# Kernel optimization log

Hardware: AMD Instinct MI355X
Metric: run time of the kernel (lower is better)

## Reference

```python
import jax, jax.numpy as jnp
import numpy as np

NUM_HEADS = 16
NUM_KV_HEADS = 8
HEAD_DIM = 128
GATE_LOW_RANK = 16
GATE_NORMALIZER = 16.0
NORM_EPS = 1e-5
CHUNK = 64


def gla_chunk(q, k, v, g, chunk=CHUNK):
    """Chunkwise-parallel gated linear attention.
    q,k,v,g: [B,H,L,D]. Recurrence: S_t = diag(exp(g_t)) S_{t-1} + k_t^T v_t; o_t = q_t S_t.
    """
    B, H, L, D = q.shape
    n = L // chunk

    def rs(x):  # -> [n, B, H, C, D]
        return x.reshape(B, H, n, chunk, D).transpose(2, 0, 1, 3, 4)

    qc, kc, vc, gc = rs(q), rs(k), rs(v), rs(g)
    causal = jnp.tril(jnp.ones((chunk, chunk), dtype=bool))

    def step(S, inp):
        qt, kt, vt, gt = inp                      # [B,H,C,D]
        b = jnp.cumsum(gt, axis=-2)               # inclusive cumulative log-gates
        q_ = qt * jnp.exp(b)
        k_ = kt * jnp.exp(-b)
        # intra-chunk causal attention (diag included)
        A = jnp.einsum('bhid,bhjd->bhij', q_, k_)
        A = jnp.where(causal, A, 0.0)
        o = jnp.einsum('bhij,bhje->bhie', A, vt)
        # inter-chunk contribution from carried state
        o = o + jnp.einsum('bhid,bhde->bhie', q_, S)
        # state update to end of chunk
        k_end = kt * jnp.exp(b[..., -1:, :] - b)
        S_new = S * jnp.exp(b[..., -1, :])[..., None] + jnp.einsum('bhcd,bhce->bhde', k_end, vt)
        return S_new, o

    S0 = jnp.zeros((B, H, D, D), q.dtype)
    _, o = jax.lax.scan(step, S0, (qc, kc, vc, gc))
    return o.transpose(1, 2, 0, 3, 4).reshape(B, H, L, D)


def setup_inputs() -> dict:
    key = jax.random.key(0)
    ks = jax.random.split(key, 10)
    B, L, HID = 2, 2048, 2048
    KV = NUM_KV_HEADS * HEAD_DIM  # 1024
    w = 0.02
    return {
        'hidden_states': jax.random.normal(ks[0], (B, L, HID), jnp.float32),
        'Wq': jax.random.normal(ks[1], (HID, HID), jnp.float32) * w,
        'bq': jnp.zeros((HID,), jnp.float32),
        'Wk': jax.random.normal(ks[2], (HID, KV), jnp.float32) * w,
        'bk': jnp.zeros((KV,), jnp.float32),
        'Wv': jax.random.normal(ks[3], (HID, KV), jnp.float32) * w,
        'bv': jnp.zeros((KV,), jnp.float32),
        'Wg1': jax.random.normal(ks[4], (HID, GATE_LOW_RANK), jnp.float32) * w,
        'Wg2': jax.random.normal(ks[5], (GATE_LOW_RANK, KV), jnp.float32) * w,
        'bg2': jnp.zeros((KV,), jnp.float32),
        'g_norm_w': jnp.ones((HEAD_DIM,), jnp.float32),
        'Wo': jax.random.normal(ks[6], (HID, HID), jnp.float32) * w,
    }


def reference(hidden_states, Wq, bq, Wk, bk, Wv, bv, Wg1, Wg2, bg2, g_norm_w, Wo):
    B, L, HID = hidden_states.shape
    H, HKV, D = NUM_HEADS, NUM_KV_HEADS, HEAD_DIM
    n_rep = H // HKV

    q = jax.nn.relu(hidden_states @ Wq + bq)          # feature_map = relu
    k = jax.nn.relu(hidden_states @ Wk + bk)
    v = hidden_states @ Wv + bv
    gk = jax.nn.log_sigmoid((hidden_states @ Wg1) @ Wg2 + bg2) / GATE_NORMALIZER

    q = q.reshape(B, L, H, D).transpose(0, 2, 1, 3)    # [B,H,L,D]
    def to_heads(x):
        return x.reshape(B, L, HKV, D).transpose(0, 2, 1, 3)
    k, v, gk = to_heads(k), to_heads(v), to_heads(gk)  # [B,HKV,L,D]
    # GQA: repeat kv heads
    k = jnp.repeat(k, n_rep, axis=1)
    v = jnp.repeat(v, n_rep, axis=1)
    gk = jnp.repeat(gk, n_rep, axis=1)

    q = q * (D ** -0.5)                                # scale as in chunk_gla
    o = gla_chunk(q, k, v, gk)                         # [B,H,L,D]

    # per-head RMSNorm over head_dim
    o = o * jax.lax.rsqrt(jnp.mean(o * o, axis=-1, keepdims=True) + NORM_EPS) * g_norm_w
    o = o.transpose(0, 2, 1, 3).reshape(B, L, H * D)
    return o @ Wo
```

## Files before the change

### kernel.cpp

```cpp
#include <hip/hip_runtime.h>

typedef unsigned short u16;
typedef u16 u16x8 __attribute__((ext_vector_type(8)));
typedef u16 u16x4 __attribute__((ext_vector_type(4)));
typedef __bf16 bf16x8 __attribute__((ext_vector_type(8)));
typedef float f32x4 __attribute__((ext_vector_type(4)));

#define DEVI static __device__ __forceinline__

DEVI float b2f(u16 u){ union { unsigned u; float f; } c; c.u = ((unsigned)u) << 16; return c.f; }
DEVI u16 f2b(float f){ union { float f; unsigned u; } c; c.f = f;
  unsigned r = c.u + 0x7fffu + ((c.u >> 16) & 1u); return (u16)(r >> 16); }
DEVI void gload16(const void* g, void* l){
  __builtin_amdgcn_global_load_lds((const __attribute__((address_space(1))) void*)g,
                                   (__attribute__((address_space(3))) void*)l, 16, 0, 0);
}
DEVI f32x4 MFMA(bf16x8 a, bf16x8 b, f32x4 c){
  return __builtin_amdgcn_mfma_f32_16x16x32_bf16(a, b, c, 0, 0, 0);
}

constexpr size_t OFF_HB  = 0;
constexpr size_t OFF_WCT = OFF_HB  + (size_t)4096*2048*2;
constexpr size_t OFF_WOT = OFF_WCT + (size_t)4224*2048*2;
constexpr size_t OFF_QKV = OFF_WOT + (size_t)2048*2048*2;
constexpr size_t OFF_G1  = OFF_QKV + (size_t)4096*4096*2;
constexpr size_t OFF_G   = OFF_G1  + (size_t)4096*16*4;
constexpr size_t OFF_EB  = OFF_G   + (size_t)4096*1024*4;
constexpr size_t OFF_KD  = OFF_EB  + (size_t)4096*1024*2;
constexpr size_t OFF_T   = OFF_KD  + (size_t)4096*1024*2;
constexpr size_t OFF_DV  = OFF_T   + (size_t)2*8*32*128*128*2;
constexpr size_t OFF_SP  = OFF_DV  + (size_t)2*8*32*128*4;
constexpr size_t OFF_ON  = OFF_SP  + (size_t)2*8*32*128*128*2;

__global__ __launch_bounds__(256) void k_conv_h(const float* __restrict__ h, u16* __restrict__ hb){
  int idx = blockIdx.x*256 + threadIdx.x, stride = gridDim.x*256;
  for (int i = idx; i < 4096*2048/4; i += stride){
    float4 v = ((const float4*)h)[i];
    u16x4 o; o[0]=f2b(v.x); o[1]=f2b(v.y); o[2]=f2b(v.z); o[3]=f2b(v.w);
    ((u16x4*)hb)[i] = o;
  }
}

__global__ __launch_bounds__(256) void k_transpose(const float* __restrict__ src, u16* __restrict__ dst,
                                                   int K, int N, int rowOff, int pitch){
  __shared__ float tile[64][65];
  int kb = blockIdx.y*64, nb = blockIdx.x*64;
  int t = threadIdx.x, x = t & 63, y0 = t >> 6;
#pragma unroll
  for (int i = 0; i < 16; i++){
    int y = y0 + i*4, k = kb + y, n = nb + x;
    tile[y][x] = (n < N) ? src[(size_t)k*N + n] : 0.f;
  }
  __syncthreads();
#pragma unroll
  for (int i = 0; i < 16; i++){
    int y = y0 + i*4, n = nb + y, k = kb + x;
    if (n < N) dst[(size_t)(rowOff + n)*pitch + k] = f2b(tile[x][y]);
  }
}

__global__ __launch_bounds__(256) void k_wtilde(const float* __restrict__ Wg1, const float* __restrict__ Wg2,
                                                u16* __restrict__ wt){
  __shared__ float w2s[16*8];
  int c0 = blockIdx.x*8, t = threadIdx.x;
  if (t < 128){ int j = t>>3, cc = t&7; w2s[j*8+cc] = Wg2[j*1024 + c0 + cc]; }
  __syncthreads();
  int r0 = t*8;
#pragma unroll
  for (int half = 0; half < 2; half++){
    float rowv[4][16];
#pragma unroll
    for (int u = 0; u < 4; u++)
#pragma unroll
      for (int j4 = 0; j4 < 4; j4++)
        *(float4*)&rowv[u][j4*4] = *(const float4*)&Wg1[(size_t)(r0 + half*4 + u)*16 + j4*4];
#pragma unroll
    for (int cc = 0; cc < 8; cc++){
      u16x4 o;
#pragma unroll
      for (int u = 0; u < 4; u++){
        float s = 0.f;
#pragma unroll
        for (int j = 0; j < 16; j++) s += rowv[u][j]*w2s[j*8+cc];
        o[u] = f2b(s);
      }
      *(u16x4*)&wt[(size_t)(c0+cc)*2048 + r0 + half*4] = o;
    }
  }
}

template<int MODE>
__global__ __launch_bounds__(256, 4) void gemm128(const u16* __restrict__ A, const u16* __restrict__ Bt,
                                                  u16* __restrict__ Cq, float* __restrict__ Cf,
                                                  const float* __restrict__ bq, const float* __restrict__ bk,
                                                  const float* __restrict__ bv, const float* __restrict__ bg2){
  constexpr int NT = 64;
  constexpr int NTN = (MODE==0) ? 32 : (MODE==1) ? 16 : 8;
  constexpr int CPX = (MODE==0) ? 128 : (MODE==1) ? 64 : 32;
  __shared__ u16 sA[2*128*32];
  __shared__ u16 sB[2*128*32];
  int id = blockIdx.x;
  int swz = (id & 7)*CPX + (id >> 3);
  int mt = swz / NTN, nt = swz % NTN;
  int t = threadIdx.x, w = t >> 6, l = t & 63;
  int wr = w >> 1, wc = w & 1;
  int mRow0 = mt*128, nCol0 = nt*128;
  const u16* srcA[2]; const u16* srcB[2];
#pragma unroll
  for (int i = 0; i < 2; i++){
    int S = t + i*256, r = S>>2, g = (S&3) ^ ((r>>1)&3);
    srcA[i] = A + (size_t)(mRow0 + r)*2048 + g*8;
    srcB[i] = Bt + (size_t)(nCol0 + r)*2048 + g*8;
  }
  auto ISSUE = [&](int T){
    int buf = T & 1;
    u16* dA = sA + buf*4096;
    u16* dB = sB + buf*4096;
#pragma unroll
    for (int i = 0; i < 2; i++) gload16(srcA[i] + T*32, dA + (i*256 + w*64)*8);
#pragma unroll
    for (int i = 0; i < 2; i++) gload16(srcB[i] + T*32, dB + (i*256 + w*64)*8);
  };
  f32x4 acc[4][4] = {};
  ISSUE(0);
  for (int T = 0; T < NT; ++T){
    __syncthreads();
    if (T + 1 < NT) ISSUE(T + 1);
    const u16* bufA = sA + (T&1)*4096;
    const u16* bufB = sB + (T&1)*4096;
    bf16x8 bfr[4], afr[4];
#pragma unroll
    for (int ni = 0; ni < 4; ni++){
      int r = wc*64 + ni*16 + (l&15);
      int p = (l>>4) ^ ((r>>1)&3);
      bfr[ni] = *(const bf16x8*)&bufB[(r*4 + p)*8];
    }
#pragma unroll
    for (int mi = 0; mi < 4; mi++){
      int r = wr*64 + mi*16 + (l&15);
      int p = (l>>4) ^ ((r>>1)&3);
      afr[mi] = *(const bf16x8*)&bufA[(r*4 + p)*8];
    }
    __builtin_amdgcn_s_setprio(1);
#pragma unroll
    for (int mi = 0; mi < 4; mi++)
#pragma unroll
      for (int ni = 0; ni < 4; ni++)
        acc[mi][ni] = MFMA(afr[mi], bfr[ni], acc[mi][ni]);
    __builtin_amdgcn_s_setprio(0);
  }
  int iLoc = (l>>4)*4, jc = l & 15;
  if (MODE == 0){
    int kind = (nt < 16) ? 0 : (nt < 24) ? 1 : 2;
#pragma unroll
    for (int ni = 0; ni < 4; ni++){
      int n = nCol0 + wc*64 + ni*16 + jc;
      float bias = (kind == 0) ? bq[n] : (kind == 1) ? bk[n - 2048] : bv[n - 3072];
#pragma unroll
      for (int mi = 0; mi < 4; mi++){
        int m = mRow0 + wr*64 + mi*16 + iLoc;
#pragma unroll
        for (int rr = 0; rr < 4; rr++){
          float x = acc[mi][ni][rr] + bias;
          int row = m + rr;
          if (kind == 0)      Cq[(size_t)row*4096 + n] = f2b(fmaxf(x, 0.f) * 0.08838834764831845f);
          else if (kind == 1) Cq[(size_t)row*4096 + n] = f2b(fmaxf(x, 0.f));
          else                Cq[(size_t)row*4096 + n] = f2b(x);
        }
      }
    }
  } else if (MODE == 1){
#pragma unroll
    for (int ni = 0; ni < 4; ni++){
      int n = nCol0 + wc*64 + ni*16 + jc;
#pragma unroll
      for (int mi = 0; mi < 4; mi++){
        int m = mRow0 + wr*64 + mi*16 + iLoc;
#pragma unroll
        for (int rr = 0; rr < 4; rr++) Cf[(size_t)(m+rr)*2048 + n] = acc[mi][ni][rr];
      }
    }
  } else {
#pragma unroll
    for (int ni = 0; ni < 4; ni++){
      int n = nCol0 + wc*64 + ni*16 + jc;
      float bias = bg2[n];
#pragma unroll
      for (int mi = 0; mi < 4; mi++){
        int m = mRow0 + wr*64 + mi*16 + iLoc;
#pragma unroll
        for (int rr = 0; rr < 4; rr++) Cf[(size_t)(m+rr)*1024 + n] = acc[mi][ni][rr] + bias;
      }
    }
  }
}

__global__ __launch_bounds__(256) void k_phaseA(const float* __restrict__ g, const u16* __restrict__ QKV,
                                                u16* __restrict__ eb, u16* __restrict__ kd,
                                                u16* __restrict__ T, float* __restrict__ Dv){
  __shared__ float gb[64*128];
  __shared__ u16 keT[128*72];
  __shared__ u16 vT [128*72];
  int c = blockIdx.x, kvh = blockIdx.y, b = blockIdx.z;
  int t = threadIdx.x;
  int tok0 = b*2048 + c*64;
#pragma unroll
  for (int r = 0; r < 8; r++){
    int idx4 = r*256 + t;
    int i = idx4 >> 5, c4 = idx4 & 31;
    float4 v = *(const float4*)&g[(size_t)(tok0+i)*1024 + kvh*128 + c4*4];
    float4 o;
    o.x = (fminf(v.x,0.f) - log1pf(expf(-fabsf(v.x)))) * 0.0625f;
    o.y = (fminf(v.y,0.f) - log1pf(expf(-fabsf(v.y)))) * 0.0625f;
    o.z = (fminf(v.z,0.f) - log1pf(expf(-fabsf(v.z)))) * 0.0625f;
    o.w = (fminf(v.w,0.f) - log1pf(expf(-fabsf(v.w)))) * 0.0625f;
    ((float4*)gb)[i*32 + c4] = o;
  }
  __syncthreads();
  if (t < 128){
    float run = 0.f;
    for (int i = 0; i < 64; i++){ run += gb[i*128 + t]; gb[i*128 + t] = run; }
    Dv[((size_t)(b*8+kvh)*32 + c)*128 + t] = expf(run);
  }
  __syncthreads();
  int d0 = (t&15)*8;
  float blast[8];
#pragma unroll
  for (int j = 0; j < 8; j++) blast[j] = gb[63*128 + d0 + j];
#pragma unroll
  for (int r = 0; r < 4; r++){
    int i = (t>>4) + r*16;
    u16x8 kv_ = *(const u16x8*)&QKV[(size_t)(tok0+i)*4096 + 2048 + kvh*128 + d0];
    u16x8 vv  = *(const u16x8*)&QKV[(size_t)(tok0+i)*4096 + 3072 + kvh*128 + d0];
    u16x8 ebv, kdv;
#pragma unroll
    for (int j = 0; j < 8; j++){
      float bcur = gb[i*128 + d0 + j];
      float kf = b2f(kv_[j]);
      ebv[j] = f2b(expf(bcur));
      kdv[j] = f2b(kf * expf(-bcur));
      keT[(d0+j)*72 + i] = f2b(kf * expf(blast[j] - bcur));
      vT [(d0+j)*72 + i] = vv[j];
    }
    *(u16x8*)&eb[(size_t)(tok0+i)*1024 + kvh*128 + d0] = ebv;
    *(u16x8*)&kd[(size_t)(tok0+i)*1024 + kvh*128 + d0] = kdv;
  }
  __syncthreads();
  int w = t>>6, l = t&63;
  f32x4 acc[2][8] = {};
#pragma unroll
  for (int ks = 0; ks < 2; ks++){
    bf16x8 af[2];
#pragma unroll
    for (int te = 0; te < 2; te++)
      af[te] = *(const bf16x8*)&vT[(w*32 + te*16 + (l&15))*72 + ks*32 + (l>>4)*8];
#pragma unroll
    for (int td = 0; td < 8; td++){
      bf16x8 bf_ = *(const bf16x8*)&keT[(td*16 + (l&15))*72 + ks*32 + (l>>4)*8];
#pragma unroll
      for (int te = 0; te < 2; te++) acc[te][td] = MFMA(af[te], bf_, acc[te][td]);
    }
  }
  size_t tbase = ((size_t)(b*8+kvh)*32 + c)*16384;
#pragma unroll
  for (int te = 0; te < 2; te++)
#pragma unroll
    for (int td = 0; td < 8; td++)
#pragma unroll
      for (int rr = 0; rr < 4; rr++){
        int e = w*32 + te*16 + (l>>4)*4 + rr, d = td*16 + (l&15);
        T[tbase + e*128 + d] = f2b(acc[te][td][rr]);
      }
}

__global__ __launch_bounds__(256) void k_phaseB(const u16* __restrict__ T, const float* __restrict__ Dv,
                                                u16* __restrict__ SP){
  int kvh = blockIdx.y, b = blockIdx.z;
  int t = threadIdx.x;
  int e = blockIdx.x*16 + (t >> 4);
  int d0 = (t & 15)*8;
  size_t base = ((size_t)(b*8 + kvh)*32)*16384 + (size_t)e*128 + d0;
  size_t dvb  = ((size_t)(b*8 + kvh)*32)*128 + d0;
  float S[8] = {0,0,0,0,0,0,0,0};
  for (int c = 0; c < 32; c++){
    u16x8 tv = *(const u16x8*)&T[base + (size_t)c*16384];
    float4 dva = *(const float4*)&Dv[dvb + (size_t)c*128];
    float4 dvbv = *(const float4*)&Dv[dvb + (size_t)c*128 + 4];
    u16x8 o;
#pragma unroll
    for (int j = 0; j < 8; j++) o[j] = f2b(S[j]);
    *(u16x8*)&SP[base + (size_t)c*16384] = o;
    float dv[8] = {dva.x, dva.y, dva.z, dva.w, dvbv.x, dvbv.y, dvbv.z, dvbv.w};
#pragma unroll
    for (int j = 0; j < 8; j++) S[j] = S[j]*dv[j] + b2f(tv[j]);
  }
}

__global__ __launch_bounds__(256) void k_phaseC(const u16* __restrict__ QKV, const u16* __restrict__ eb,
                                                const u16* __restrict__ kd, const u16* __restrict__ SP,
                                                const float* __restrict__ gnw, u16* __restrict__ onrm){
  __shared__ u16 kl[64*128];
  __shared__ u16 sl[64*72];
  __shared__ u16 vT[128*72];
  int c = blockIdx.x, h = blockIdx.y, b = blockIdx.z;
  int kvh = h >> 1;
  int t = threadIdx.x, w = t>>6, l = t&63;
  int tok0 = b*2048 + c*64;
#pragma unroll
  for (int is = 0; is < 4; is++){
    int row = (t>>4) + is*16;
    int d0s = 8*((t&15) ^ (row&7));
    gload16(&kd[(size_t)(tok0+row)*1024 + kvh*128 + d0s], &kl[is*2048 + w*512]);
  }
  int d0v = (t&15)*8;
#pragma unroll
  for (int r = 0; r < 4; r++){
    int i = (t>>4) + r*16;
    u16x8 vv = *(const u16x8*)&QKV[(size_t)(tok0+i)*4096 + 3072 + kvh*128 + d0v];
#pragma unroll
    for (int jj = 0; jj < 8; jj++) vT[(d0v+jj)*72 + i] = vv[jj];
  }
  bf16x8 aq[4];
  {
    int i = w*16 + (l&15);
#pragma unroll
    for (int kt = 0; kt < 4; kt++){
      int dq = kt*32 + (l>>4)*8;
      u16x8 qv = *(const u16x8*)&QKV[(size_t)(tok0+i)*4096 + h*128 + dq];
      u16x8 ev = *(const u16x8*)&eb[(size_t)(tok0+i)*1024 + kvh*128 + dq];
      u16x8 o;
#pragma unroll
      for (int jj = 0; jj < 8; jj++) o[jj] = f2b(b2f(qv[jj]) * b2f(ev[jj]));
      aq[kt] = __builtin_bit_cast(bf16x8, o);
    }
  }
  __syncthreads();
  f32x4 accs[4] = {};
#pragma unroll
  for (int kt = 0; kt < 4; kt++){
#pragma unroll
    for (int jt = 0; jt < 4; jt++){
      int j = jt*16 + (l&15);
      int byte_ = j*256 + ((2*(kt*32 + (l>>4)*8)) ^ ((j&7)<<4));
      bf16x8 bk_ = *(const bf16x8*)((const char*)kl + byte_);
      accs[jt] = MFMA(aq[kt], bk_, accs[jt]);
    }
  }
#pragma unroll
  for (int jt = 0; jt < 4; jt++)
#pragma unroll
    for (int rr = 0; rr < 4; rr++){
      int i = w*16 + (l>>4)*4 + rr;
      int j = jt*16 + (l&15);
      sl[i*72 + j] = f2b((i >= j) ? accs[jt][rr] : 0.f);
    }
  f32x4 acco[8] = {};
  size_t spb = ((size_t)(b*8+kvh)*32 + c)*16384;
#pragma unroll
  for (int kt = 0; kt < 4; kt++){
#pragma unroll
    for (int et = 0; et < 8; et++){
      int e = et*16 + (l&15);
      int dd = kt*32 + (l>>4)*8;
      bf16x8 bs = *(const bf16x8*)&SP[spb + (size_t)e*128 + dd];
      acco[et] = MFMA(aq[kt], bs, acco[et]);
    }
  }
#pragma unroll
  for (int kt2 = 0; kt2 < 2; kt2++){
    int i = w*16 + (l&15);
    bf16x8 as = *(const bf16x8*)&sl[i*72 + kt2*32 + (l>>4)*8];
#pragma unroll
    for (int et = 0; et < 8; et++){
      bf16x8 bv_ = *(const bf16x8*)&vT[(et*16 + (l&15))*72 + kt2*32 + (l>>4)*8];
      acco[et] = MFMA(as, bv_, acco[et]);
    }
  }
  float gw[8];
#pragma unroll
  for (int et = 0; et < 8; et++) gw[et] = gnw[et*16 + (l&15)];
#pragma unroll
  for (int rr = 0; rr < 4; rr++){
    int i = w*16 + (l>>4)*4 + rr;
    float ss = 0.f;
#pragma unroll
    for (int et = 0; et < 8; et++){ float x = acco[et][rr]; ss += x*x; }
    ss += __shfl_xor(ss, 1); ss += __shfl_xor(ss, 2);
    ss += __shfl_xor(ss, 4); ss += __shfl_xor(ss, 8);
    float sc = rsqrtf(ss*(1.f/128.f) + 1e-5f);
#pragma unroll
    for (int et = 0; et < 8; et++){
      int e = et*16 + (l&15);
      onrm[(size_t)(tok0+i)*2048 + h*128 + e] = f2b(acco[et][rr]*sc*gw[et]);
    }
  }
}

extern "C" void kernel_launch(void* const* d_in, const int* in_sizes, int n_in,
                              void* d_out, int out_size, void* d_ws, size_t ws_size,
                              hipStream_t stream){
  (void)in_sizes; (void)n_in; (void)out_size; (void)ws_size;
  const float* h   = (const float*)d_in[0];
  const float* Wq  = (const float*)d_in[1];
  const float* bq  = (const float*)d_in[2];
  const float* Wk  = (const float*)d_in[3];
  const float* bk  = (const float*)d_in[4];
  const float* Wv  = (const float*)d_in[5];
  const float* bv  = (const float*)d_in[6];
  const float* Wg1 = (const float*)d_in[7];
  const float* Wg2 = (const float*)d_in[8];
  const float* bg2 = (const float*)d_in[9];
  const float* gnw = (const float*)d_in[10];
  const float* Wo  = (const float*)d_in[11];
  float* out = (float*)d_out;
  char* ws = (char*)d_ws;
  u16*   hb   = (u16*)  (ws + OFF_HB);
  u16*   wct  = (u16*)  (ws + OFF_WCT);
  u16*   wot  = (u16*)  (ws + OFF_WOT);
  u16*   qkv  = (u16*)  (ws + OFF_QKV);
  float* gbuf = (float*)(ws + OFF_G);
  u16*   ebuf = (u16*)  (ws + OFF_EB);
  u16*   kdb  = (u16*)  (ws + OFF_KD);
  u16*   Tb   = (u16*)  (ws + OFF_T);
  u16*   wtilT= (u16*)  (ws + OFF_T);
  float* Dvb  = (float*)(ws + OFF_DV);
  u16*   SPb  = (u16*)  (ws + OFF_SP);
  u16*   onb  = (u16*)  (ws + OFF_ON);

  k_conv_h<<<2048, 256, 0, stream>>>(h, hb);
  k_transpose<<<dim3(32,32), 256, 0, stream>>>(Wq,  wct, 2048, 2048,    0, 2048);
  k_transpose<<<dim3(16,32), 256, 0, stream>>>(Wk,  wct, 2048, 1024, 2048, 2048);
  k_transpose<<<dim3(16,32), 256, 0, stream>>>(Wv,  wct, 2048, 1024, 3072, 2048);
  k_transpose<<<dim3(32,32), 256, 0, stream>>>(Wo,  wot, 2048, 2048,    0, 2048);
  k_wtilde<<<128, 256, 0, stream>>>(Wg1, Wg2, wtilT);
  gemm128<0><<<1024, 256, 0, stream>>>(hb, wct, qkv, nullptr, bq, bk, bv, nullptr);
  gemm128<2><<<256, 256, 0, stream>>>(hb, wtilT, nullptr, gbuf, nullptr, nullptr, nullptr, bg2);
  k_phaseA<<<dim3(32,8,2), 256, 0, stream>>>(gbuf, qkv, ebuf, kdb, Tb, Dvb);
  k_phaseB<<<dim3(8,8,2), 256, 0, stream>>>(Tb, Dvb, SPb);
  k_phaseC<<<dim3(32,16,2), 256, 0, stream>>>(qkv, ebuf, kdb, SPb, gnw, onb);
  gemm128<1><<<512, 256, 0, stream>>>(onb, wot, nullptr, out, nullptr, nullptr, nullptr, nullptr);
}
```

Before: 423.0 us.

## Fuse prep kernels, merge gate GEMM into QKV GEMM, share K/V across head pairs

Merges the bf16 conversion, the four weight transposes and the low-rank gate weight build into a single prep launch. Folds the gate projection GEMM into the QKV GEMM by adding extra N tiles that read from a separate weight buffer and write fp32 gates with bias. phaseC now runs one block per KV head and loops over both query heads, so the K/V tiles staged in shared memory are reused, at the cost of half as many blocks and extra barriers. Two serial loops also get unroll pragmas. The intent is fewer launches, better GEMM occupancy and less redundant K/V loading.

```diff
diff --git a/kernel.cpp b/kernel.cpp
--- a/kernel.cpp
+++ b/kernel.cpp
@@ -31,38 +31,48 @@
 constexpr size_t OFF_DV  = OFF_T   + (size_t)2*8*32*128*128*2;
 constexpr size_t OFF_SP  = OFF_DV  + (size_t)2*8*32*128*4;
 constexpr size_t OFF_ON  = OFF_SP  + (size_t)2*8*32*128*128*2;
-
-__global__ __launch_bounds__(256) void k_conv_h(const float* __restrict__ h, u16* __restrict__ hb){
-  int idx = blockIdx.x*256 + threadIdx.x, stride = gridDim.x*256;
-  for (int i = idx; i < 4096*2048/4; i += stride){
-    float4 v = ((const float4*)h)[i];
-    u16x4 o; o[0]=f2b(v.x); o[1]=f2b(v.y); o[2]=f2b(v.z); o[3]=f2b(v.w);
-    ((u16x4*)hb)[i] = o;
-  }
-}
-
-__global__ __launch_bounds__(256) void k_transpose(const float* __restrict__ src, u16* __restrict__ dst,
-                                                   int K, int N, int rowOff, int pitch){
+constexpr size_t OFF_WTL = OFF_ON  + (size_t)4096*2048*2;
+
+__global__ __launch_bounds__(256) void k_prep(const float* __restrict__ h, u16* __restrict__ hb,
+                                              const float* __restrict__ Wq, const float* __restrict__ Wk,
+                                              const float* __restrict__ Wv, const float* __restrict__ Wo,
+                                              u16* __restrict__ wct, u16* __restrict__ wot,
+                                              const float* __restrict__ Wg1, const float* __restrict__ Wg2,
+                                              u16* __restrict__ wt){
   __shared__ float tile[64][65];
-  int kb = blockIdx.y*64, nb = blockIdx.x*64;
-  int t = threadIdx.x, x = t & 63, y0 = t >> 6;
-#pragma unroll
-  for (int i = 0; i < 16; i++){
-    int y = y0 + i*4, k = kb + y, n = nb + x;
-    tile[y][x] = (n < N) ? src[(size_t)k*N + n] : 0.f;
-  }
-  __syncthreads();
-#pragma unroll
-  for (int i = 0; i < 16; i++){
-    int y = y0 + i*4, n = nb + y, k = kb + x;
-    if (n < N) dst[(size_t)(rowOff + n)*pitch + k] = f2b(tile[x][y]);
-  }
-}
-
-__global__ __launch_bounds__(256) void k_wtilde(const float* __restrict__ Wg1, const float* __restrict__ Wg2,
-                                                u16* __restrict__ wt){
+  int id = blockIdx.x, t = threadIdx.x;
+  if (id < 2048){
+    int idx = id*256 + t;
+    for (int i = idx; i < 4096*2048/4; i += 2048*256){
+      float4 v = ((const float4*)h)[i];
+      u16x4 o; o[0]=f2b(v.x); o[1]=f2b(v.y); o[2]=f2b(v.z); o[3]=f2b(v.w);
+      ((u16x4*)hb)[i] = o;
+    }
+    return;
+  }
+  if (id < 5120){
+    const float* src; u16* dst; int N, rowOff, bx, by;
+    if (id < 3072){ int lo = id-2048; src = Wq; dst = wct; N = 2048; rowOff = 0;    bx = lo&31; by = lo>>5; }
+    else if (id < 3584){ int lo = id-3072; src = Wk; dst = wct; N = 1024; rowOff = 2048; bx = lo&15; by = lo>>4; }
+    else if (id < 4096){ int lo = id-3584; src = Wv; dst = wct; N = 1024; rowOff = 3072; bx = lo&15; by = lo>>4; }
+    else { int lo = id-4096; src = Wo; dst = wot; N = 2048; rowOff = 0; bx = lo&31; by = lo>>5; }
+    int kb = by*64, nb = bx*64;
+    int x = t & 63, y0 = t >> 6;
+#pragma unroll
+    for (int i = 0; i < 16; i++){
+      int y = y0 + i*4;
+      tile[y][x] = src[(size_t)(kb + y)*N + nb + x];
+    }
+    __syncthreads();
+#pragma unroll
+    for (int i = 0; i < 16; i++){
+      int y = y0 + i*4;
+      dst[(size_t)(rowOff + nb + y)*2048 + kb + x] = f2b(tile[x][y]);
+    }
+    return;
+  }
   __shared__ float w2s[16*8];
-  int c0 = blockIdx.x*8, t = threadIdx.x;
+  int c0 = (id - 5120)*8;
   if (t < 128){ int j = t>>3, cc = t&7; w2s[j*8+cc] = Wg2[j*1024 + c0 + cc]; }
   __syncthreads();
   int r0 = t*8;
@@ -91,12 +101,13 @@
 
 template<int MODE>
 __global__ __launch_bounds__(256, 4) void gemm128(const u16* __restrict__ A, const u16* __restrict__ Bt,
+                                                  const u16* __restrict__ BtHi,
                                                   u16* __restrict__ Cq, float* __restrict__ Cf,
                                                   const float* __restrict__ bq, const float* __restrict__ bk,
                                                   const float* __restrict__ bv, const float* __restrict__ bg2){
   constexpr int NT = 64;
-  constexpr int NTN = (MODE==0) ? 32 : (MODE==1) ? 16 : 8;
-  constexpr int CPX = (MODE==0) ? 128 : (MODE==1) ? 64 : 32;
+  constexpr int NTN = (MODE==0) ? 40 : 16;
+  constexpr int CPX = (MODE==0) ? 160 : 64;
   __shared__ u16 sA[2*128*32];
   __shared__ u16 sB[2*128*32];
   int id = blockIdx.x;
@@ -105,12 +116,14 @@
   int t = threadIdx.x, w = t >> 6, l = t & 63;
   int wr = w >> 1, wc = w & 1;
   int mRow0 = mt*128, nCol0 = nt*128;
+  const u16* Bbase = (MODE==0 && nCol0 >= 4096) ? (BtHi + (size_t)(nCol0-4096)*2048)
+                                                : (Bt + (size_t)nCol0*2048);
   const u16* srcA[2]; const u16* srcB[2];
 #pragma unroll
   for (int i = 0; i < 2; i++){
     int S = t + i*256, r = S>>2, g = (S&3) ^ ((r>>1)&3);
     srcA[i] = A + (size_t)(mRow0 + r)*2048 + g*8;
-    srcB[i] = Bt + (size_t)(nCol0 + r)*2048 + g*8;
+    srcB[i] = Bbase + (size_t)r*2048 + g*8;
   }
   auto ISSUE = [&](int T){
     int buf = T & 1;
@@ -151,11 +164,12 @@
   }
   int iLoc = (l>>4)*4, jc = l & 15;
   if (MODE == 0){
-    int kind = (nt < 16) ? 0 : (nt < 24) ? 1 : 2;
+    int kind = (nt < 16) ? 0 : (nt < 24) ? 1 : (nt < 32) ? 2 : 3;
 #pragma unroll
     for (int ni = 0; ni < 4; ni++){
       int n = nCol0 + wc*64 + ni*16 + jc;
-      float bias = (kind == 0) ? bq[n] : (kind == 1) ? bk[n - 2048] : bv[n - 3072];
+      float bias = (kind == 0) ? bq[n] : (kind == 1) ? bk[n - 2048]
+                 : (kind == 2) ? bv[n - 3072] : bg2[n - 4096];
 #pragma unroll
       for (int mi = 0; mi < 4; mi++){
         int m = mRow0 + wr*64 + mi*16 + iLoc;
@@ -165,11 +179,12 @@
           int row = m + rr;
           if (kind == 0)      Cq[(size_t)row*4096 + n] = f2b(fmaxf(x, 0.f) * 0.08838834764831845f);
           else if (kind == 1) Cq[(size_t)row*4096 + n] = f2b(fmaxf(x, 0.f));
-          else                Cq[(size_t)row*4096 + n] = f2b(x);
+          else if (kind == 2) Cq[(size_t)row*4096 + n] = f2b(x);
+          else                Cf[(size_t)row*1024 + (n - 4096)] = x;
         }
       }
     }
-  } else if (MODE == 1){
+  } else {
 #pragma unroll
     for (int ni = 0; ni < 4; ni++){
       int n = nCol0 + wc*64 + ni*16 + jc;
@@ -178,18 +193,6 @@
         int m = mRow0 + wr*64 + mi*16 + iLoc;
 #pragma unroll
         for (int rr = 0; rr < 4; rr++) Cf[(size_t)(m+rr)*2048 + n] = acc[mi][ni][rr];
-      }
-    }
-  } else {
-#pragma unroll
-    for (int ni = 0; ni < 4; ni++){
-      int n = nCol0 + wc*64 + ni*16 + jc;
-      float bias = bg2[n];
-#pragma unroll
-      for (int mi = 0; mi < 4; mi++){
-        int m = mRow0 + wr*64 + mi*16 + iLoc;
-#pragma unroll
-        for (int rr = 0; rr < 4; rr++) Cf[(size_t)(m+rr)*1024 + n] = acc[mi][ni][rr] + bias;
       }
     }
   }
@@ -219,6 +222,7 @@
   __syncthreads();
   if (t < 128){
     float run = 0.f;
+#pragma unroll
     for (int i = 0; i < 64; i++){ run += gb[i*128 + t]; gb[i*128 + t] = run; }
     Dv[((size_t)(b*8+kvh)*32 + c)*128 + t] = expf(run);
   }
@@ -282,6 +286,7 @@
   size_t base = ((size_t)(b*8 + kvh)*32)*16384 + (size_t)e*128 + d0;
   size_t dvb  = ((size_t)(b*8 + kvh)*32)*128 + d0;
   float S[8] = {0,0,0,0,0,0,0,0};
+#pragma unroll 4
   for (int c = 0; c < 32; c++){
     u16x8 tv = *(const u16x8*)&T[base + (size_t)c*16384];
     float4 dva = *(const float4*)&Dv[dvb + (size_t)c*128];
@@ -302,8 +307,7 @@
   __shared__ u16 kl[64*128];
   __shared__ u16 sl[64*72];
   __shared__ u16 vT[128*72];
-  int c = blockIdx.x, h = blockIdx.y, b = blockIdx.z;
-  int kvh = h >> 1;
+  int c = blockIdx.x, kvh = blockIdx.y, b = blockIdx.z;
   int t = threadIdx.x, w = t>>6, l = t&63;
   int tok0 = b*2048 + c*64;
 #pragma unroll
@@ -320,79 +324,92 @@
 #pragma unroll
     for (int jj = 0; jj < 8; jj++) vT[(d0v+jj)*72 + i] = vv[jj];
   }
-  bf16x8 aq[4];
+  u16x8 evv[4];
   {
     int i = w*16 + (l&15);
 #pragma unroll
     for (int kt = 0; kt < 4; kt++){
       int dq = kt*32 + (l>>4)*8;
-      u16x8 qv = *(const u16x8*)&QKV[(size_t)(tok0+i)*4096 + h*128 + dq];
-      u16x8 ev = *(const u16x8*)&eb[(size_t)(tok0+i)*1024 + kvh*128 + dq];
-      u16x8 o;
-#pragma unroll
-      for (int jj = 0; jj < 8; jj++) o[jj] = f2b(b2f(qv[jj]) * b2f(ev[jj]));
-      aq[kt] = __builtin_bit_cast(bf16x8, o);
-    }
-  }
+      evv[kt] = *(const u16x8*)&eb[(size_t)(tok0+i)*1024 + kvh*128 + dq];
+    }
+  }
+  float gw[8];
+#pragma unroll
+  for (int et = 0; et < 8; et++) gw[et] = gnw[et*16 + (l&15)];
+  size_t spb = ((size_t)(b*8+kvh)*32 + c)*16384;
   __syncthreads();
-  f32x4 accs[4] = {};
-#pragma unroll
-  for (int kt = 0; kt < 4; kt++){
-#pragma unroll
-    for (int jt = 0; jt < 4; jt++){
-      int j = jt*16 + (l&15);
-      int byte_ = j*256 + ((2*(kt*32 + (l>>4)*8)) ^ ((j&7)<<4));
-      bf16x8 bk_ = *(const bf16x8*)((const char*)kl + byte_);
-      accs[jt] = MFMA(aq[kt], bk_, accs[jt]);
-    }
-  }
-#pragma unroll
-  for (int jt = 0; jt < 4; jt++)
+  for (int h2 = 0; h2 < 2; h2++){
+    int h = kvh*2 + h2;
+    bf16x8 aq[4];
+    {
+      int i = w*16 + (l&15);
+#pragma unroll
+      for (int kt = 0; kt < 4; kt++){
+        int dq = kt*32 + (l>>4)*8;
+        u16x8 qv = *(const u16x8*)&QKV[(size_t)(tok0+i)*4096 + h*128 + dq];
+        u16x8 o;
+#pragma unroll
+        for (int jj = 0; jj < 8; jj++) o[jj] = f2b(b2f(qv[jj]) * b2f(evv[kt][jj]));
+        aq[kt] = __builtin_bit_cast(bf16x8, o);
+      }
+    }
+    f32x4 accs[4] = {};
+#pragma unroll
+    for (int kt = 0; kt < 4; kt++){
+#pragma unroll
+      for (int jt = 0; jt < 4; jt++){
+        int j = jt*16 + (l&15);
+        int byte_ = j*256 + ((2*(kt*32 + (l>>4)*8)) ^ ((j&7)<<4));
+        bf16x8 bk_ = *(const bf16x8*)((const char*)kl + byte_);
+        accs[jt] = MFMA(aq[kt], bk_, accs[jt]);
+      }
+    }
+#pragma unroll
+    for (int jt = 0; jt < 4; jt++)
+#pragma unroll
+      for (int rr = 0; rr < 4; rr++){
+        int i = w*16 + (l>>4)*4 + rr;
+        int j = jt*16 + (l&15);
+        sl[i*72 + j] = f2b((i >= j) ? accs[jt][rr] : 0.f);
+      }
+    f32x4 acco[8] = {};
+#pragma unroll
+    for (int kt = 0; kt < 4; kt++){
+#pragma unroll
+      for (int et = 0; et < 8; et++){
+        int e = et*16 + (l&15);
+        int dd = kt*32 + (l>>4)*8;
+        bf16x8 bs = *(const bf16x8*)&SP[spb + (size_t)e*128 + dd];
+        acco[et] = MFMA(aq[kt], bs, acco[et]);
+      }
+    }
+    __syncthreads();
+#pragma unroll
+    for (int kt2 = 0; kt2 < 2; kt2++){
+      int i = w*16 + (l&15);
+      bf16x8 as = *(const bf16x8*)&sl[i*72 + kt2*32 + (l>>4)*8];
+#pragma unroll
+      for (int et = 0; et < 8; et++){
+        bf16x8 bv_ = *(const bf16x8*)&vT[(et*16 + (l&15))*72 + kt2*32 + (l>>4)*8];
+        acco[et] = MFMA(as, bv_, acco[et]);
+      }
+    }
 #pragma unroll
     for (int rr = 0; rr < 4; rr++){
       int i = w*16 + (l>>4)*4 + rr;
-      int j = jt*16 + (l&15);
-      sl[i*72 + j] = f2b((i >= j) ? accs[jt][rr] : 0.f);
-    }
-  f32x4 acco[8] = {};
-  size_t spb = ((size_t)(b*8+kvh)*32 + c)*16384;
-#pragma unroll
-  for (int kt = 0; kt < 4; kt++){
-#pragma unroll
-    for (int et = 0; et < 8; et++){
-      int e = et*16 + (l&15);
-      int dd = kt*32 + (l>>4)*8;
-      bf16x8 bs = *(const bf16x8*)&SP[spb + (size_t)e*128 + dd];
-      acco[et] = MFMA(aq[kt], bs, acco[et]);
-    }
-  }
-#pragma unroll
-  for (int kt2 = 0; kt2 < 2; kt2++){
-    int i = w*16 + (l&15);
-    bf16x8 as = *(const bf16x8*)&sl[i*72 + kt2*32 + (l>>4)*8];
-#pragma unroll
-    for (int et = 0; et < 8; et++){
-      bf16x8 bv_ = *(const bf16x8*)&vT[(et*16 + (l&15))*72 + kt2*32 + (l>>4)*8];
-      acco[et] = MFMA(as, bv_, acco[et]);
-    }
-  }
-  float gw[8];
-#pragma unroll
-  for (int et = 0; et < 8; et++) gw[et] = gnw[et*16 + (l&15)];
-#pragma unroll
-  for (int rr = 0; rr < 4; rr++){
-    int i = w*16 + (l>>4)*4 + rr;
-    float ss = 0.f;
-#pragma unroll
-    for (int et = 0; et < 8; et++){ float x = acco[et][rr]; ss += x*x; }
-    ss += __shfl_xor(ss, 1); ss += __shfl_xor(ss, 2);
-    ss += __shfl_xor(ss, 4); ss += __shfl_xor(ss, 8);
-    float sc = rsqrtf(ss*(1.f/128.f) + 1e-5f);
-#pragma unroll
-    for (int et = 0; et < 8; et++){
-      int e = et*16 + (l&15);
-      onrm[(size_t)(tok0+i)*2048 + h*128 + e] = f2b(acco[et][rr]*sc*gw[et]);
-    }
+      float ss = 0.f;
+#pragma unroll
+      for (int et = 0; et < 8; et++){ float x = acco[et][rr]; ss += x*x; }
+      ss += __shfl_xor(ss, 1); ss += __shfl_xor(ss, 2);
+      ss += __shfl_xor(ss, 4); ss += __shfl_xor(ss, 8);
+      float sc = rsqrtf(ss*(1.f/128.f) + 1e-5f);
+#pragma unroll
+      for (int et = 0; et < 8; et++){
+        int e = et*16 + (l&15);
+        onrm[(size_t)(tok0+i)*2048 + h*128 + e] = f2b(acco[et][rr]*sc*gw[et]);
+      }
+    }
+    __syncthreads();
   }
 }
 
@@ -422,21 +439,15 @@
   u16*   ebuf = (u16*)  (ws + OFF_EB);
   u16*   kdb  = (u16*)  (ws + OFF_KD);
   u16*   Tb   = (u16*)  (ws + OFF_T);
-  u16*   wtilT= (u16*)  (ws + OFF_T);
   float* Dvb  = (float*)(ws + OFF_DV);
   u16*   SPb  = (u16*)  (ws + OFF_SP);
   u16*   onb  = (u16*)  (ws + OFF_ON);
-
-  k_conv_h<<<2048, 256, 0, stream>>>(h, hb);
-  k_transpose<<<dim3(32,32), 256, 0, stream>>>(Wq,  wct, 2048, 2048,    0, 2048);
-  k_transpose<<<dim3(16,32), 256, 0, stream>>>(Wk,  wct, 2048, 1024, 2048, 2048);
-  k_transpose<<<dim3(16,32), 256, 0, stream>>>(Wv,  wct, 2048, 1024, 3072, 2048);
-  k_transpose<<<dim3(32,32), 256, 0, stream>>>(Wo,  wot, 2048, 2048,    0, 2048);
-  k_wtilde<<<128, 256, 0, stream>>>(Wg1, Wg2, wtilT);
-  gemm128<0><<<1024, 256, 0, stream>>>(hb, wct, qkv, nullptr, bq, bk, bv, nullptr);
-  gemm128<2><<<256, 256, 0, stream>>>(hb, wtilT, nullptr, gbuf, nullptr, nullptr, nullptr, bg2);
+  u16*   wtilT= (u16*)  (ws + OFF_WTL);
+
+  k_prep<<<5248, 256, 0, stream>>>(h, hb, Wq, Wk, Wv, Wo, wct, wot, Wg1, Wg2, wtilT);
+  gemm128<0><<<1280, 256, 0, stream>>>(hb, wct, wtilT, qkv, gbuf, bq, bk, bv, bg2);
   k_phaseA<<<dim3(32,8,2), 256, 0, stream>>>(gbuf, qkv, ebuf, kdb, Tb, Dvb);
   k_phaseB<<<dim3(8,8,2), 256, 0, stream>>>(Tb, Dvb, SPb);
-  k_phaseC<<<dim3(32,16,2), 256, 0, stream>>>(qkv, ebuf, kdb, SPb, gnw, onb);
-  gemm128<1><<<512, 256, 0, stream>>>(onb, wot, nullptr, out, nullptr, nullptr, nullptr, nullptr);
-}
+  k_phaseC<<<dim3(32,8,2), 256, 0, stream>>>(qkv, ebuf, kdb, SPb, gnw, onb);
+  gemm128<1><<<512, 256, 0, stream>>>(onb, wot, nullptr, nullptr, out, nullptr, nullptr, nullptr, nullptr);
+}
```

Result: faster. 406.0 us (-4.0%).
